# Optimization experiments

Measured on AMD Instinct MI355X. Metric: run time of the kernel, lower is better.

Reference implementation:

```python
import jax, jax.numpy as jnp
import numpy as np

H_Q, H_KV, D_HEAD = 32, 4, 128

def setup_inputs() -> dict:
    key = jax.random.key(0)
    ks = jax.random.split(key, 5)
    B, S, H = 1, 4096, 2048
    hidden_states = jax.random.normal(ks[0], (B, S, H), jnp.float32)
    Wq = jax.random.normal(ks[1], (H, H_Q * D_HEAD), jnp.float32) * 0.02
    Wk = jax.random.normal(ks[2], (H, H_KV * D_HEAD), jnp.float32) * 0.02
    Wv = jax.random.normal(ks[3], (H, H_KV * D_HEAD), jnp.float32) * 0.02
    Wo = jax.random.normal(ks[4], (H_Q * D_HEAD, H), jnp.float32) * 0.02
    position_ids = jnp.arange(S, dtype=jnp.int32)
    # causal boolean mask, used as-is by the layer when rank != 2
    attention_mask = jnp.tril(jnp.ones((S, S), dtype=bool))[None, None]
    return dict(hidden_states=hidden_states, Wq=Wq, Wk=Wk, Wv=Wv, Wo=Wo,
                position_ids=position_ids, attention_mask=attention_mask)

def _rope(x, positions):
    # x: [B, S, H, D]; rotate-half style RoPE, max_wavelength=10000, scaling=1
    d = x.shape[-1]
    inv_freq = 1.0 / (10000.0 ** (jnp.arange(0, d, 2, dtype=jnp.float32) / d))  # [d/2]
    freq = positions.astype(jnp.float32)[:, None] * inv_freq[None, :]           # [S, d/2]
    emb = jnp.concatenate([freq, freq], axis=-1)                                # [S, d]
    cos = jnp.cos(emb)[None, :, None, :]
    sin = jnp.sin(emb)[None, :, None, :]
    x1, x2 = jnp.split(x, 2, axis=-1)
    rot = jnp.concatenate([-x2, x1], axis=-1)
    return x * cos + rot * sin

def reference(hidden_states, Wq, Wk, Wv, Wo, position_ids, attention_mask):
    B, S, H = hidden_states.shape
    q = (hidden_states @ Wq).reshape(B, S, H_Q, D_HEAD)
    k = (hidden_states @ Wk).reshape(B, S, H_KV, D_HEAD)
    v = (hidden_states @ Wv).reshape(B, S, H_KV, D_HEAD)
    q = _rope(q, position_ids)
    k = _rope(k, position_ids)
    q = q.transpose(0, 2, 1, 3)                                   # [B,Hq,S,D]
    num_groups = H_Q // H_KV
    k = jnp.repeat(k.transpose(0, 2, 1, 3), num_groups, axis=1)   # [B,Hq,S,D]
    v = jnp.repeat(v.transpose(0, 2, 1, 3), num_groups, axis=1)
    scores = jnp.einsum('bhqd,bhkd->bhqk', q, k) / jnp.sqrt(jnp.float32(D_HEAD))
    scores = jnp.where(attention_mask, scores, jnp.float32(-1e9))
    weights = jax.nn.softmax(scores, axis=-1)
    out = jnp.einsum('bhqk,bhkd->bhqd', weights, v)
    out = out.transpose(0, 2, 1, 3).reshape(B, S, H_Q * D_HEAD)
    return out @ Wo
```

## Files before the change

### kernel.cpp

```cpp
#include <hip/hip_runtime.h>
#include <hip/hip_bf16.h>

typedef __attribute__((ext_vector_type(8))) short bf16x8;
typedef __attribute__((ext_vector_type(4))) float f32x4;
typedef __attribute__((ext_vector_type(16))) float f32x16;

#define WAIT_VMCNT(n) asm volatile("s_waitcnt vmcnt(" #n ")" ::: "memory")
#define WAIT_LGKM0()  asm volatile("s_waitcnt lgkmcnt(0)" ::: "memory")

__device__ __forceinline__ unsigned short f2b(float f) {
  __hip_bfloat16 h = __float2bfloat16(f);
  return __builtin_bit_cast(unsigned short, h);
}
__device__ __forceinline__ float b2f(unsigned short u) {
  return __bfloat162float(__builtin_bit_cast(__hip_bfloat16, u));
}
__device__ __forceinline__ unsigned int pk2(float a, float b) {
  unsigned int r;
  asm("v_cvt_pk_bf16_f32 %0, %1, %2" : "=v"(r) : "v"(a), "v"(b));
  return r;
}

__device__ __forceinline__ void gld_lds16(const void* g, void* l) {
  __builtin_amdgcn_global_load_lds(
      (const __attribute__((address_space(1))) unsigned int*)g,
      (__attribute__((address_space(3))) unsigned int*)l, 16, 0, 0);
}

__global__ void convert_kernel(const float* __restrict__ in, unsigned short* __restrict__ out, int n4) {
  int i = blockIdx.x * blockDim.x + threadIdx.x;
  if (i >= n4) return;
  float4 v = ((const float4*)in)[i];
  uint2 o;
  o.x = pk2(v.x, v.y);
  o.y = pk2(v.z, v.w);
  *(uint2*)(out + (size_t)i * 4) = o;
}

__global__ void transpose_convert_kernel(const float* __restrict__ in, unsigned short* __restrict__ out,
                                         int R, int C) {
  __shared__ float tile[32][33];
  int c0 = blockIdx.x * 32, r0 = blockIdx.y * 32;
  int tx = threadIdx.x, ty = threadIdx.y;
#pragma unroll
  for (int k = 0; k < 32; k += 8)
    tile[ty + k][tx] = in[(size_t)(r0 + ty + k) * C + (c0 + tx)];
  __syncthreads();
#pragma unroll
  for (int k = 0; k < 32; k += 8)
    out[(size_t)(c0 + ty + k) * R + (r0 + tx)] = f2b(tile[tx][ty + k]);
}

__global__ void rope_kernel(unsigned short* __restrict__ buf, const int* __restrict__ pos,
                            int log2h, int rowstride, float outscale, int total) {
  int idx = blockIdx.x * blockDim.x + threadIdx.x;
  if (idx >= total) return;
  int i = idx & 63;
  int h = (idx >> 6) & ((1 << log2h) - 1);
  int s = idx >> (6 + log2h);
  float inv = expf(-0.14391156831212787f * (float)i);
  float f = (float)pos[s] * inv;
  float sn, cs;
  sincosf(f, &sn, &cs);
  unsigned short* p = buf + (size_t)s * rowstride + (h << 7) + i;
  float x1 = b2f(p[0]);
  float x2 = b2f(p[64]);
  p[0]  = f2b((x1 * cs - x2 * sn) * outscale);
  p[64] = f2b((x2 * cs + x1 * sn) * outscale);
}

template <int OUT_MODE, int BM, int BN>
__global__ __launch_bounds__(512, 2) void gemm_big_kernel(const unsigned short* __restrict__ A,
                                                          const unsigned short* __restrict__ Bt,
                                                          void* __restrict__ Cv,
                                                          int M, int N, int K) {
  constexpr int MI = BM / 32;
  constexpr int WN = BN / 4;
  constexpr int NI = WN / 16;
  constexpr int A_IT = BM / 64;
  constexpr int B_IT = BN / 64;
  __shared__ unsigned short As[2][BM * 64];
  __shared__ unsigned short Bs[2][BN * 64];

  int tid = threadIdx.x, lane = tid & 63, wave = tid >> 6;
  int wm = wave >> 2, wn = wave & 3;

  int gx = gridDim.x, nwg = gx * gridDim.y;
  int lin = blockIdx.y * gx + blockIdx.x;
  int swz = (lin & 7) * (nwg >> 3) + (lin >> 3);
  int m0 = (swz / gx) * BM, n0 = (swz % gx) * BN;

  int row0 = tid >> 3, ch = tid & 7;
  const unsigned short* pa0 = A + (size_t)(m0 + row0) * K + ((ch ^ (row0 & 7)) << 3);
  const unsigned short* pb0 = Bt + (size_t)(n0 + row0) * K + ((ch ^ (row0 & 7)) << 3);
  size_t rstep = (size_t)64 * K;

  auto stage = [&](int b, int kt) {
    const unsigned short* a = pa0 + (size_t)kt * 64;
    const unsigned short* bb = pb0 + (size_t)kt * 64;
#pragma unroll
    for (int it = 0; it < A_IT; ++it)
      gld_lds16(a + it * rstep, (unsigned short*)As[b] + (it * 512 + tid) * 8);
#pragma unroll
    for (int it = 0; it < B_IT; ++it)
      gld_lds16(bb + it * rstep, (unsigned short*)Bs[b] + (it * 512 + tid) * 8);
  };

  f32x4 acc[MI][NI] = {};

  int nk = K >> 6;
  stage(0, 0);
  stage(1, 1);
  for (int kt = 0; kt < nk; ++kt) {
    int cur = kt & 1;
    if (kt + 1 < nk) {
      if constexpr (A_IT + B_IT == 8) WAIT_VMCNT(8);
      else if constexpr (A_IT + B_IT == 6) WAIT_VMCNT(6);
      else WAIT_VMCNT(4);
    } else {
      WAIT_VMCNT(0);
    }
    __builtin_amdgcn_s_barrier();

    bf16x8 af[MI][2], bfr[NI][2];
#pragma unroll
    for (int mi = 0; mi < MI; ++mi) {
      int r = wm * (BM / 2) + mi * 16 + (lane & 15);
#pragma unroll
      for (int kk = 0; kk < 2; ++kk)
        af[mi][kk] = *(const bf16x8*)((const char*)As[cur] +
                      r * 128 + (((kk * 4 + (lane >> 4)) ^ (r & 7)) << 4));
    }
#pragma unroll
    for (int ni = 0; ni < NI; ++ni) {
      int r = wn * WN + ni * 16 + (lane & 15);
#pragma unroll
      for (int kk = 0; kk < 2; ++kk)
        bfr[ni][kk] = *(const bf16x8*)((const char*)Bs[cur] +
                       r * 128 + (((kk * 4 + (lane >> 4)) ^ (r & 7)) << 4));
    }
    WAIT_LGKM0();
    __builtin_amdgcn_s_barrier();
    if (kt + 2 < nk) stage(cur, kt + 2);

    __builtin_amdgcn_s_setprio(1);
#pragma unroll
    for (int mi = 0; mi < MI; ++mi)
#pragma unroll
      for (int ni = 0; ni < NI; ++ni)
#pragma unroll
        for (int kk = 0; kk < 2; ++kk)
          acc[mi][ni] = __builtin_amdgcn_mfma_f32_16x16x32_bf16(af[mi][kk], bfr[ni][kk],
                                                                acc[mi][ni], 0, 0, 0);
    __builtin_amdgcn_s_setprio(0);
  }

#pragma unroll
  for (int mi = 0; mi < MI; ++mi) {
#pragma unroll
    for (int ni = 0; ni < NI; ++ni) {
      int col = n0 + wn * WN + ni * 16 + (lane & 15);
      int rbase = m0 + wm * (BM / 2) + mi * 16 + (lane >> 4) * 4;
#pragma unroll
      for (int j = 0; j < 4; ++j) {
        if (OUT_MODE == 1)
          ((float*)Cv)[(size_t)(rbase + j) * N + col] = acc[mi][ni][j];
        else
          ((unsigned short*)Cv)[(size_t)(rbase + j) * N + col] = f2b(acc[mi][ni][j]);
      }
    }
  }
}

__global__ __launch_bounds__(256) void gemm_kv_kernel(const unsigned short* __restrict__ A,
                                                      const unsigned short* __restrict__ Bt,
                                                      unsigned short* __restrict__ Kb,
                                                      unsigned short* __restrict__ Vt,
                                                      int K) {
  __shared__ unsigned short As[3][128 * 32];
  __shared__ unsigned short Bs[3][128 * 32];
  int tid = threadIdx.x;
  int lane = tid & 63;
  int wave = tid >> 6;

  int nwg = gridDim.x * gridDim.y;
  int lin = blockIdx.y * gridDim.x + blockIdx.x;
  int cpx = nwg >> 3;
  int swz = (lin & 7) * cpx + (lin >> 3);
  int m0 = (swz / gridDim.x) * 128, n0 = (swz % gridDim.x) * 128;

  int wr = wave >> 1, wc = wave & 1;
  f32x4 acc[4][4] = {};

  int row0 = tid >> 2, cc0 = tid & 3;
  const unsigned short* pa0 = A + (size_t)(m0 + row0) * K + cc0 * 8;
  const unsigned short* pa1 = A + (size_t)(m0 + row0 + 64) * K + cc0 * 8;
  const unsigned short* pb0 = Bt + (size_t)(n0 + row0) * K + cc0 * 8;
  const unsigned short* pb1 = Bt + (size_t)(n0 + row0 + 64) * K + cc0 * 8;

  auto stage = [&](int b, int k0) {
    gld_lds16(pa0 + k0, (unsigned short*)As[b] + tid * 8);
    gld_lds16(pa1 + k0, (unsigned short*)As[b] + (256 + tid) * 8);
    gld_lds16(pb0 + k0, (unsigned short*)Bs[b] + tid * 8);
    gld_lds16(pb1 + k0, (unsigned short*)Bs[b] + (256 + tid) * 8);
  };

  int nk = K >> 5;
  stage(0, 0);
  stage(1, 32);
  int cur = 0;
  for (int ki = 0; ki < nk; ++ki) {
    if (ki + 1 < nk) WAIT_VMCNT(4); else WAIT_VMCNT(0);
    __builtin_amdgcn_s_barrier();
    if (ki + 2 < nk) {
      int b2 = cur + 2; if (b2 >= 3) b2 -= 3;
      stage(b2, (ki + 2) * 32);
    }
    bf16x8 af[4], bfr[4];
#pragma unroll
    for (int mi = 0; mi < 4; ++mi) {
      int r = wr * 64 + mi * 16 + (lane & 15);
      af[mi] = *(const bf16x8*)((const char*)As[cur] + r * 64 + (lane >> 4) * 16);
    }
#pragma unroll
    for (int ni = 0; ni < 4; ++ni) {
      int r = wc * 64 + ni * 16 + (lane & 15);
      bfr[ni] = *(const bf16x8*)((const char*)Bs[cur] + r * 64 + (lane >> 4) * 16);
    }
#pragma unroll
    for (int mi = 0; mi < 4; ++mi)
#pragma unroll
      for (int ni = 0; ni < 4; ++ni)
        acc[mi][ni] = __builtin_amdgcn_mfma_f32_16x16x32_bf16(af[mi], bfr[ni], acc[mi][ni], 0, 0, 0);
    cur = (cur == 2) ? 0 : cur + 1;
  }

#pragma unroll
  for (int mi = 0; mi < 4; ++mi) {
#pragma unroll
    for (int ni = 0; ni < 4; ++ni) {
      int col = n0 + wc * 64 + ni * 16 + (lane & 15);
      int rbase = m0 + wr * 64 + mi * 16 + (lane >> 4) * 4;
      if (col < 512) {
#pragma unroll
        for (int j = 0; j < 4; ++j)
          Kb[(size_t)(rbase + j) * 512 + col] = f2b(acc[mi][ni][j]);
      } else {
        int cv = col - 512;
        int hk = cv >> 7, d = cv & 127;
        uint2 u;
        u.x = pk2(acc[mi][ni][0], acc[mi][ni][1]);
        u.y = pk2(acc[mi][ni][2], acc[mi][ni][3]);
        size_t addr = (size_t)hk * 524288 + (size_t)(rbase >> 6) * 8192 + d * 64 + (rbase & 63);
        *(uint2*)(Vt + addr) = u;
      }
    }
  }
}

__global__ __launch_bounds__(512) void attn_kernel(const unsigned short* __restrict__ Q,
                                                   const unsigned short* __restrict__ Kp,
                                                   const unsigned short* __restrict__ Vt,
                                                   unsigned short* __restrict__ O) {
  __shared__ unsigned short k_lds[4][64 * 128];
  __shared__ unsigned short vt_lds[4][128 * 64];

  int lin = blockIdx.y * 8 + blockIdx.x;
  int h = (lin & 7) * 4 + (lin >> 6);
  int xpair = (lin >> 3) & 7;
  int hk = h >> 3;
  int tid = threadIdx.x, lane = tid & 63, wave = tid >> 6;
  int l31 = lane & 31, hi = lane >> 5;

  int krow0 = tid >> 4, kch = tid & 15;
  int krow1 = krow0 + 32;
  const unsigned short* kp0 = Kp + (hk << 7) + (size_t)krow0 * 512 + ((kch ^ (krow0 & 15)) << 3);
  const unsigned short* kp1 = Kp + (hk << 7) + (size_t)krow1 * 512 + ((kch ^ (krow1 & 15)) << 3);
  int vd0 = tid >> 3, vsc = tid & 7;
  int vd1 = vd0 + 64;
  const unsigned short* vp0 = Vt + (size_t)hk * 524288 + vd0 * 64 + ((vsc ^ (vd0 & 7)) << 3);
  const unsigned short* vp1 = Vt + (size_t)hk * 524288 + vd1 * 64 + ((vsc ^ (vd1 & 7)) << 3);

  auto stage_tile = [&](int b, int t) {
    gld_lds16(kp0 + (size_t)t * 32768, (unsigned short*)k_lds[b] + tid * 8);
    gld_lds16(kp1 + (size_t)t * 32768, (unsigned short*)k_lds[b] + (512 + tid) * 8);
    gld_lds16(vp0 + (size_t)t * 8192, (unsigned short*)vt_lds[b] + tid * 8);
    gld_lds16(vp1 + (size_t)t * 8192, (unsigned short*)vt_lds[b] + (512 + tid) * 8);
  };

  for (int pass = 0; pass < 2; ++pass) {
    int SB = pass ? (15 - xpair) : xpair;
    int qt = SB * 8 + wave;
    int qrow = qt * 32 + l31;
    int tdiag = qt >> 1;
    int ntiles = 4 * SB + 4;
    int npairs = ntiles >> 1;

    bf16x8 qf[8];
#pragma unroll
    for (int kk = 0; kk < 8; ++kk)
      qf[kk] = *(const bf16x8*)(Q + (size_t)qrow * 4096 + (h << 7) + kk * 16 + hi * 8);

    f32x16 o_acc[4] = {};
    float m_run = -3.0e38f, l_run = 0.0f;

    __syncthreads();
    stage_tile(0, 0);
    stage_tile(1, 1);
    for (int p = 0; p < npairs; ++p) {
      WAIT_VMCNT(0);
      __builtin_amdgcn_s_barrier();
      if (2 * p + 2 < ntiles) {
        stage_tile((2 * p + 2) & 3, 2 * p + 2);
        stage_tile((2 * p + 3) & 3, 2 * p + 3);
      }

#pragma unroll
      for (int half = 0; half < 2; ++half) {
        int t0 = 2 * p + half;
        int cur = t0 & 3;
        if (t0 > tdiag) continue;
        int s0 = t0 * 64;
        f32x16 sacc[2] = {};
        __builtin_amdgcn_s_setprio(1);
#pragma unroll
        for (int kk = 0; kk < 8; ++kk) {
#pragma unroll
          for (int t = 0; t < 2; ++t) {
            bf16x8 kf = *(const bf16x8*)((const char*)k_lds[cur] +
                         ((t * 32 + l31) * 256 + (((kk * 2 + hi) ^ (l31 & 15)) << 4)));
            sacc[t] = __builtin_amdgcn_mfma_f32_32x32x16_bf16(kf, qf[kk], sacc[t], 0, 0, 0);
          }
        }
        __builtin_amdgcn_s_setprio(0);

        float mx = -3.0e38f;
        if (t0 == tdiag) {
#pragma unroll
          for (int t = 0; t < 2; ++t)
#pragma unroll
            for (int r = 0; r < 16; ++r) {
              int sg = s0 + t * 32 + (r & 3) + 8 * (r >> 2) + 4 * hi;
              float v = sacc[t][r];
              v = (sg <= qrow) ? v : -3.0e38f;
              sacc[t][r] = v;
              mx = fmaxf(mx, v);
            }
        } else {
#pragma unroll
          for (int t = 0; t < 2; ++t)
#pragma unroll
            for (int r = 0; r < 16; ++r)
              mx = fmaxf(mx, sacc[t][r]);
        }
        mx = fmaxf(mx, __shfl_xor(mx, 32));
        if (!__all(mx <= m_run + 11.5416f)) {
          float m_new = fmaxf(m_run, mx);
          float corr = exp2f(m_run - m_new);
          l_run *= corr;
#pragma unroll
          for (int ds = 0; ds < 4; ++ds)
#pragma unroll
            for (int r = 0; r < 16; ++r) o_acc[ds][r] *= corr;
          m_run = m_new;
        }
        float rsum = 0.0f;
#pragma unroll
        for (int t = 0; t < 2; ++t)
#pragma unroll
          for (int r = 0; r < 16; ++r) {
            float e = exp2f(sacc[t][r] - m_run);
            sacc[t][r] = e;
            rsum += e;
          }
        l_run += rsum + __shfl_xor(rsum, 32);

        bf16x8 pb[4];
#pragma unroll
        for (int kk = 0; kk < 4; ++kk) {
          int t = kk >> 1;
          int b0 = (kk & 1) * 8;
          unsigned int a0 = pk2(sacc[t][b0 + 0], sacc[t][b0 + 1]);
          unsigned int a1 = pk2(sacc[t][b0 + 2], sacc[t][b0 + 3]);
          unsigned int c0 = pk2(sacc[t][b0 + 4], sacc[t][b0 + 5]);
          unsigned int c1 = pk2(sacc[t][b0 + 6], sacc[t][b0 + 7]);
          unsigned int snd0 = hi ? a0 : c0, snd1 = hi ? a1 : c1;
          unsigned int rcv0 = __shfl_xor(snd0, 32);
          unsigned int rcv1 = __shfl_xor(snd1, 32);
          unsigned int own0 = hi ? c0 : a0, own1 = hi ? c1 : a1;
          uint4 w;
          w.x = hi ? rcv0 : own0;
          w.y = hi ? rcv1 : own1;
          w.z = hi ? own0 : rcv0;
          w.w = hi ? own1 : rcv1;
          pb[kk] = __builtin_bit_cast(bf16x8, w);
        }

        __builtin_amdgcn_s_setprio(1);
#pragma unroll
        for (int ds = 0; ds < 4; ++ds) {
#pragma unroll
          for (int kk = 0; kk < 4; ++kk) {
            bf16x8 vf = *(const bf16x8*)((const char*)vt_lds[cur] +
                         ((ds * 32 + l31) * 128 + (((kk * 2 + hi) ^ (l31 & 7)) << 4)));
            o_acc[ds] = __builtin_amdgcn_mfma_f32_32x32x16_bf16(vf, pb[kk], o_acc[ds], 0, 0, 0);
          }
        }
        __builtin_amdgcn_s_setprio(0);
      }
    }

    __syncthreads();

    float inv_l = 1.0f / l_run;
    char* scr = (char*)k_lds + wave * 2304;
#pragma unroll
    for (int ds = 0; ds < 4; ++ds) {
#pragma unroll
      for (int rp = 0; rp < 8; ++rp) {
        int r = rp * 2;
        int d_loc = (r & 3) + 8 * (r >> 2) + 4 * hi;
        *(unsigned int*)(scr + l31 * 72 + ((d_loc >> 1) << 2)) =
            pk2(o_acc[ds][r] * inv_l, o_acc[ds][r + 1] * inv_l);
      }
      uint2 u0 = *(uint2*)(scr + l31 * 72 + hi * 32 + 0);
      uint2 u1 = *(uint2*)(scr + l31 * 72 + hi * 32 + 8);
      uint2 u2 = *(uint2*)(scr + l31 * 72 + hi * 32 + 16);
      uint2 u3 = *(uint2*)(scr + l31 * 72 + hi * 32 + 24);
      unsigned short* op = O + (size_t)qrow * 4096 + (h << 7) + ds * 32 + hi * 16;
      uint4 s0v; s0v.x = u0.x; s0v.y = u0.y; s0v.z = u1.x; s0v.w = u1.y;
      uint4 s1v; s1v.x = u2.x; s1v.y = u2.y; s1v.z = u3.x; s1v.w = u3.y;
      *(uint4*)(op) = s0v;
      *(uint4*)(op + 8) = s1v;
    }
  }
}

extern "C" void kernel_launch(void* const* d_in, const int* in_sizes, int n_in,
                              void* d_out, int out_size, void* d_ws, size_t ws_size,
                              hipStream_t stream) {
  const float* X  = (const float*)d_in[0];
  const float* Wq = (const float*)d_in[1];
  const float* Wk = (const float*)d_in[2];
  const float* Wv = (const float*)d_in[3];
  const float* Wo = (const float*)d_in[4];
  const int* pos  = (const int*)d_in[5];

  const size_t MB = 1u << 20;
  char* w = (char*)d_ws;
  unsigned short* Xb  = (unsigned short*)(w + 0 * MB);
  unsigned short* Wqt = (unsigned short*)(w + 16 * MB);
  unsigned short* Wkt = (unsigned short*)(w + 32 * MB);
  unsigned short* Wvt = (unsigned short*)(w + 34 * MB);
  unsigned short* Wot = (unsigned short*)(w + 36 * MB);
  unsigned short* Qb  = (unsigned short*)(w + 52 * MB);
  unsigned short* Kb  = (unsigned short*)(w + 84 * MB);
  unsigned short* Vtb = (unsigned short*)(w + 88 * MB);
  unsigned short* Ob  = (unsigned short*)(w + 92 * MB);

  convert_kernel<<<8192, 256, 0, stream>>>(X, Xb, 4096 * 2048 / 4);
  transpose_convert_kernel<<<dim3(128, 64), dim3(32, 8), 0, stream>>>(Wq, Wqt, 2048, 4096);
  transpose_convert_kernel<<<dim3(16, 64),  dim3(32, 8), 0, stream>>>(Wk, Wkt, 2048, 512);
  transpose_convert_kernel<<<dim3(16, 64),  dim3(32, 8), 0, stream>>>(Wv, Wvt, 2048, 512);
  transpose_convert_kernel<<<dim3(64, 128), dim3(32, 8), 0, stream>>>(Wo, Wot, 4096, 2048);

  gemm_big_kernel<0, 256, 256><<<dim3(16, 16), 512, 0, stream>>>(Xb, Wqt, Qb, 4096, 4096, 2048);
  gemm_kv_kernel<<<dim3(8, 32), 256, 0, stream>>>(Xb, Wkt, Kb, Vtb, 2048);

  rope_kernel<<<(4096 * 32 * 64) / 256, 256, 0, stream>>>(Qb, pos, 5, 4096, 0.12752792534390558f, 4096 * 32 * 64);
  rope_kernel<<<(4096 * 4 * 64) / 256,  256, 0, stream>>>(Kb, pos, 2, 512, 1.0f, 4096 * 4 * 64);

  attn_kernel<<<dim3(8, 32), 512, 0, stream>>>(Qb, Kb, Vtb, Ob);

  gemm_big_kernel<1, 128, 256><<<dim3(8, 32), 512, 0, stream>>>(Ob, Wot, d_out, 4096, 2048, 4096);
}
```

Before: 409.5 us.

## Triple-buffer big GEMM LDS stages and fix tile to 128x256

The big GEMM kernel moves from double to triple buffering in LDS. The next-next stage is issued right after the barrier, so the second barrier and the lgkmcnt wait before prefetch go away. Tile size is fixed at 128x256, so the Q projection now runs with 128-row tiles on a 16x32 grid instead of 256x256 tiles. The third buffer raises LDS use to 144KB per block, which may limit occupancy to one block per CU, and the smaller Q tile lowers data reuse.

```diff
diff --git a/kernel.cpp b/kernel.cpp
--- a/kernel.cpp
+++ b/kernel.cpp
@@ -6,7 +6,6 @@
 typedef __attribute__((ext_vector_type(16))) float f32x16;
 
 #define WAIT_VMCNT(n) asm volatile("s_waitcnt vmcnt(" #n ")" ::: "memory")
-#define WAIT_LGKM0()  asm volatile("s_waitcnt lgkmcnt(0)" ::: "memory")
 
 __device__ __forceinline__ unsigned short f2b(float f) {
   __hip_bfloat16 h = __float2bfloat16(f);
@@ -69,18 +68,16 @@
   p[64] = f2b((x2 * cs + x1 * sn) * outscale);
 }
 
-template <int OUT_MODE, int BM, int BN>
+template <int OUT_MODE>
 __global__ __launch_bounds__(512, 2) void gemm_big_kernel(const unsigned short* __restrict__ A,
                                                           const unsigned short* __restrict__ Bt,
                                                           void* __restrict__ Cv,
                                                           int M, int N, int K) {
+  constexpr int BM = 128, BN = 256;
   constexpr int MI = BM / 32;
-  constexpr int WN = BN / 4;
-  constexpr int NI = WN / 16;
-  constexpr int A_IT = BM / 64;
-  constexpr int B_IT = BN / 64;
-  __shared__ unsigned short As[2][BM * 64];
-  __shared__ unsigned short Bs[2][BN * 64];
+  constexpr int NI = 4;
+  __shared__ unsigned short As[3][BM * 64];
+  __shared__ unsigned short Bs[3][BN * 64];
 
   int tid = threadIdx.x, lane = tid & 63, wave = tid >> 6;
   int wm = wave >> 2, wn = wave & 3;
@@ -99,10 +96,10 @@
     const unsigned short* a = pa0 + (size_t)kt * 64;
     const unsigned short* bb = pb0 + (size_t)kt * 64;
 #pragma unroll
-    for (int it = 0; it < A_IT; ++it)
+    for (int it = 0; it < 2; ++it)
       gld_lds16(a + it * rstep, (unsigned short*)As[b] + (it * 512 + tid) * 8);
 #pragma unroll
-    for (int it = 0; it < B_IT; ++it)
+    for (int it = 0; it < 4; ++it)
       gld_lds16(bb + it * rstep, (unsigned short*)Bs[b] + (it * 512 + tid) * 8);
   };
 
@@ -111,16 +108,14 @@
   int nk = K >> 6;
   stage(0, 0);
   stage(1, 1);
+  int cur = 0;
   for (int kt = 0; kt < nk; ++kt) {
-    int cur = kt & 1;
-    if (kt + 1 < nk) {
-      if constexpr (A_IT + B_IT == 8) WAIT_VMCNT(8);
-      else if constexpr (A_IT + B_IT == 6) WAIT_VMCNT(6);
-      else WAIT_VMCNT(4);
-    } else {
-      WAIT_VMCNT(0);
-    }
+    if (kt + 1 < nk) WAIT_VMCNT(6); else WAIT_VMCNT(0);
     __builtin_amdgcn_s_barrier();
+    if (kt + 2 < nk) {
+      int b2 = cur + 2; if (b2 >= 3) b2 -= 3;
+      stage(b2, kt + 2);
+    }
 
     bf16x8 af[MI][2], bfr[NI][2];
 #pragma unroll
@@ -133,15 +128,12 @@
     }
 #pragma unroll
     for (int ni = 0; ni < NI; ++ni) {
-      int r = wn * WN + ni * 16 + (lane & 15);
+      int r = wn * 64 + ni * 16 + (lane & 15);
 #pragma unroll
       for (int kk = 0; kk < 2; ++kk)
         bfr[ni][kk] = *(const bf16x8*)((const char*)Bs[cur] +
                        r * 128 + (((kk * 4 + (lane >> 4)) ^ (r & 7)) << 4));
     }
-    WAIT_LGKM0();
-    __builtin_amdgcn_s_barrier();
-    if (kt + 2 < nk) stage(cur, kt + 2);
 
     __builtin_amdgcn_s_setprio(1);
 #pragma unroll
@@ -153,13 +145,14 @@
           acc[mi][ni] = __builtin_amdgcn_mfma_f32_16x16x32_bf16(af[mi][kk], bfr[ni][kk],
                                                                 acc[mi][ni], 0, 0, 0);
     __builtin_amdgcn_s_setprio(0);
+    cur = (cur == 2) ? 0 : cur + 1;
   }
 
 #pragma unroll
   for (int mi = 0; mi < MI; ++mi) {
 #pragma unroll
     for (int ni = 0; ni < NI; ++ni) {
-      int col = n0 + wn * WN + ni * 16 + (lane & 15);
+      int col = n0 + wn * 64 + ni * 16 + (lane & 15);
       int rbase = m0 + wm * (BM / 2) + mi * 16 + (lane >> 4) * 4;
 #pragma unroll
       for (int j = 0; j < 4; ++j) {
@@ -464,7 +457,7 @@
   transpose_convert_kernel<<<dim3(16, 64),  dim3(32, 8), 0, stream>>>(Wv, Wvt, 2048, 512);
   transpose_convert_kernel<<<dim3(64, 128), dim3(32, 8), 0, stream>>>(Wo, Wot, 4096, 2048);
 
-  gemm_big_kernel<0, 256, 256><<<dim3(16, 16), 512, 0, stream>>>(Xb, Wqt, Qb, 4096, 4096, 2048);
+  gemm_big_kernel<0><<<dim3(16, 32), 512, 0, stream>>>(Xb, Wqt, Qb, 4096, 4096, 2048);
   gemm_kv_kernel<<<dim3(8, 32), 256, 0, stream>>>(Xb, Wkt, Kb, Vtb, 2048);
 
   rope_kernel<<<(4096 * 32 * 64) / 256, 256, 0, stream>>>(Qb, pos, 5, 4096, 0.12752792534390558f, 4096 * 32 * 64);
@@ -472,5 +465,5 @@
 
   attn_kernel<<<dim3(8, 32), 512, 0, stream>>>(Qb, Kb, Vtb, Ob);
 
-  gemm_big_kernel<1, 128, 256><<<dim3(8, 32), 512, 0, stream>>>(Ob, Wot, d_out, 4096, 2048, 4096);
-}
+  gemm_big_kernel<1><<<dim3(8, 32), 512, 0, stream>>>(Ob, Wot, d_out, 4096, 2048, 4096);
+}
```

Measured after the change: 446.3 us. 9.0% more time.
